# Performance work log

Measured on AMD Instinct MI355X. Metric: run time of the kernel, lower is better.

## Reference

```python
import jax, jax.numpy as jnp
import numpy as np

BN_EPS = 1e-5


def _get_normals(radius, nsample, xyz):
    # xyz: [B, N, 3] -> normals [B, N, 3] (eigenvector of smallest eigenvalue)
    B, N, _ = xyz.shape
    sq = jnp.sum(xyz * xyz, axis=-1)                      # [B, N]
    sqrdists = sq[:, :, None] + sq[:, None, :] - 2.0 * jnp.einsum('bnc,bmc->bnm', xyz, xyz)
    ar = jnp.arange(N, dtype=jnp.int32)
    group_idx = jnp.where(sqrdists > radius * radius, N, ar[None, None, :])  # [B, N, N]
    group_idx = jnp.sort(group_idx, axis=-1)[:, :, :nsample]                 # [B, N, ns]
    group_idx = jnp.where(group_idx == N, group_idx[:, :, :1], group_idx)
    group_points = jax.vmap(lambda pts, idx: pts[idx])(xyz, group_idx)       # [B, N, ns, 3]
    centered = group_points - group_points.mean(axis=2, keepdims=True)
    cov = jnp.einsum('bnsc,bnsd->bncd', centered, centered)                  # [B, N, 3, 3]
    _, eigen_vectors = jnp.linalg.eigh(cov)
    return eigen_vectors[..., 0]


def _conv_bn(h, w, b, g, be, m, v, relu=True):
    # h: [B, N, Cin]; 1x1 Conv1d == per-point linear; BN in eval mode
    h = h @ w.T + b
    h = (h - m) / jnp.sqrt(v + BN_EPS) * g + be
    return jax.nn.relu(h) if relu else h


def setup_inputs() -> dict:
    key = jax.random.key(0)
    ks = jax.random.split(key, 32)
    B, N = 4, 4096
    inp = {
        'x': jax.random.uniform(ks[0], (B, N, 3), dtype=jnp.float32),
        'small': 0.2,
        'large': 0.3,
    }
    chans = [(1, 16), (16, 32), (32, 16), (16, 1)]
    for li, (cin, cout) in enumerate(chans, start=1):
        k = 4 * li
        inp[f'w{li}'] = jax.random.normal(ks[k], (cout, cin), dtype=jnp.float32) * (1.0 / np.sqrt(cin))
        inp[f'b{li}'] = jax.random.normal(ks[k + 1], (cout,), dtype=jnp.float32) * 0.1
        inp[f'g{li}'] = jax.random.uniform(ks[k + 2], (cout,), dtype=jnp.float32) + 0.5
        inp[f'be{li}'] = jax.random.normal(ks[k + 3], (cout,), dtype=jnp.float32) * 0.1
        inp[f'm{li}'] = jnp.zeros((cout,), dtype=jnp.float32)
        inp[f'v{li}'] = jnp.ones((cout,), dtype=jnp.float32)
    return inp


def reference(x, small, large,
              w1, b1, g1, be1, m1, v1,
              w2, b2, g2, be2, m2, v2,
              w3, b3, g3, be3, m3, v3,
              w4, b4, g4, be4, m4, v4):
    xyz = x[:, :, :3]
    small_n = _get_normals(small, 32, xyz)   # [B, N, 3]
    large_n = _get_normals(large, 64, xyz)
    curvature = jnp.linalg.norm((small_n - large_n) * 0.5, axis=2)  # [B, N]
    h = curvature[..., None]                                        # [B, N, 1]
    h = _conv_bn(h, w1, b1, g1, be1, m1, v1)
    h = _conv_bn(h, w2, b2, g2, be2, m2, v2)
    h = _conv_bn(h, w3, b3, g3, be3, m3, v3)
    h = _conv_bn(h, w4, b4, g4, be4, m4, v4, relu=False)
    return h[..., 0]                                                # [B, N]
```

## Files before the change

kernel.cpp:

```cpp
#include <hip/hip_runtime.h>
#include <math.h>

#define BLAS_FMA 1
#define SYR2_VARIANT 0

#define DEV static __device__ __forceinline__

DEV float fA(float a, float b){ return __fadd_rn(a,b); }
DEV float fSb(float a, float b){ return __fsub_rn(a,b); }
DEV float fM(float a, float b){ return __fmul_rn(a,b); }
DEV float fDv(float a, float b){ return __fdiv_rn(a,b); }
DEV float fQ(float a){ return __fsqrt_rn(a); }
DEV float fF(float a, float b, float c){ return __builtin_fmaf(a,b,c); }
DEV float fSGN(float a, float b){ return copysignf(a,b); }

DEV float slapy2f(float x, float y){
  float xa=fabsf(x), ya=fabsf(y);
  float w=fmaxf(xa,ya), z=fminf(xa,ya);
  if (z==0.0f) return w;
  float t=fDv(z,w);
  return fM(w, fQ(fA(1.0f, fM(t,t))));
}

DEV void slartgf(float f, float g, float* c, float* s, float* r){
  const float safmin=1.17549435e-38f;
  const float safmax=8.50705917e+37f;
  const float rtmin=1.08420217e-19f;
  const float rtmax=6.52169543e+18f;
  float f1=fabsf(f), g1=fabsf(g);
  if (g==0.0f){ *c=1.0f; *s=0.0f; *r=f; }
  else if (f==0.0f){ *c=0.0f; *s=fSGN(1.0f,g); *r=g1; }
  else {
    if (f1>rtmin && f1<rtmax && g1>rtmin && g1<rtmax){
      float d=fQ(fA(fM(f,f), fM(g,g)));
      *c=fDv(f1,d);
      *r=fSGN(d,f);
      *s=fDv(g,*r);
    } else {
      float u=fminf(safmax, fmaxf(safmin, fmaxf(f1,g1)));
      float fs=fDv(f,u), gs=fDv(g,u);
      float d=fQ(fA(fM(fs,fs), fM(gs,gs)));
      *c=fDv(fabsf(fs), d);
      *r=fSGN(d,f);
      *s=fDv(gs,*r);
      *r=fM(*r,u);
    }
  }
}

DEV void slaev2f(float a, float b, float c, float* rt1, float* rt2, float* cs1, float* sn1){
  float sm=fA(a,c);
  float df=fSb(a,c);
  float adf=fabsf(df);
  float tb=fA(b,b);
  float ab=fabsf(tb);
  float acmx, acmn;
  if (fabsf(a)>fabsf(c)){ acmx=a; acmn=c; } else { acmx=c; acmn=a; }
  float rt;
  if (adf>ab){ float t=fDv(ab,adf); rt=fM(adf, fQ(fA(1.0f, fM(t,t)))); }
  else if (adf<ab){ float t=fDv(adf,ab); rt=fM(ab, fQ(fA(1.0f, fM(t,t)))); }
  else { rt=fM(ab, fQ(2.0f)); }
  int sgn1;
  if (sm<0.0f){
    *rt1=fM(0.5f, fSb(sm,rt)); sgn1=-1;
    *rt2=fSb(fM(fDv(acmx,*rt1),acmn), fM(fDv(b,*rt1),b));
  } else if (sm>0.0f){
    *rt1=fM(0.5f, fA(sm,rt)); sgn1=1;
    *rt2=fSb(fM(fDv(acmx,*rt1),acmn), fM(fDv(b,*rt1),b));
  } else {
    *rt1=fM(0.5f,rt); *rt2=fM(-0.5f,rt); sgn1=1;
  }
  float cs; int sgn2;
  if (df>=0.0f){ cs=fA(df,rt); sgn2=1; } else { cs=fSb(df,rt); sgn2=-1; }
  float acs=fabsf(cs);
  if (acs>ab){
    float ct=fDv(-tb,cs);
    *sn1=fDv(1.0f, fQ(fA(1.0f, fM(ct,ct))));
    *cs1=fM(ct,*sn1);
  } else {
    if (ab==0.0f){ *cs1=1.0f; *sn1=0.0f; }
    else {
      float tn=fDv(-cs,tb);
      *cs1=fDv(1.0f, fQ(fA(1.0f, fM(tn,tn))));
      *sn1=fM(tn,*cs1);
    }
  }
  if (sgn1==sgn2){ float tn=*cs1; *cs1=-(*sn1); *sn1=tn; }
}

DEV void eig3_smallest(float a00, float a10, float a20, float a11, float a21, float a22,
                       float* vout){
  const float RMIN=3.13916472e-16f;
  const float RMAX=3.18559313e+15f;
  float anrm=fmaxf(fabsf(a00), fmaxf(fabsf(a10), fmaxf(fabsf(a20),
             fmaxf(fabsf(a11), fmaxf(fabsf(a21), fabsf(a22))))));
  if (anrm>0.0f && anrm<RMIN){
    float sig=fDv(RMIN,anrm);
    a00=fM(a00,sig); a10=fM(a10,sig); a20=fM(a20,sig);
    a11=fM(a11,sig); a21=fM(a21,sig); a22=fM(a22,sig);
  } else if (anrm>RMAX){
    float sig=fDv(RMAX,anrm);
    a00=fM(a00,sig); a10=fM(a10,sig); a20=fM(a20,sig);
    a11=fM(a11,sig); a21=fM(a21,sig); a22=fM(a22,sig);
  }
  float d[3], e[2];
  float tau1=0.0f, hv2=0.0f;
  {
    float xnorm=fabsf(a20);
    if (xnorm==0.0f){
      tau1=0.0f;
      d[0]=a00; d[1]=a11; d[2]=a22;
      e[0]=a10; e[1]=a21;
    } else {
      float alpha=a10;
      float beta=-fSGN(slapy2f(alpha,xnorm), alpha);
      tau1=fDv(fSb(beta,alpha), beta);
      float rs=fDv(1.0f, fSb(alpha,beta));
      hv2=fM(a20, rs);
      float t2a=fM(a21, hv2);
#if BLAS_FMA
      float w1=fF(tau1, t2a, fM(tau1, a11));
      float w2=fF(fM(tau1,hv2), a22, fM(tau1, a21));
      float sd=fF(hv2, w2, w1);
#else
      float w1=fA(fM(tau1,a11), fM(tau1,t2a));
      float w2=fA(fM(tau1,a21), fM(fM(tau1,hv2),a22));
      float sd=fA(w1, fM(w2,hv2));
#endif
      float al2=fM(fM(-0.5f,tau1), sd);
      float nw1=fA(w1, al2);
#if BLAS_FMA
      float nw2=fF(al2, hv2, w2);
#else
      float nw2=fA(w2, fM(al2,hv2));
#endif
      w1=nw1; w2=nw2;
      float b11, b21, b22;
#if SYR2_VARIANT==0
      b11=fA(a11, fM(-2.0f, w1));
      b21=fA(a21, fF(hv2, -w1, -w2));
      b22=fA(a22, fF(hv2, -w2, fM(w2, -hv2)));
#elif SYR2_VARIANT==1
      b11=fSb(fSb(a11, w1), w1);
      b21=fSb(fF(hv2, -w1, a21), w2);
      b22=fF(w2, -hv2, fF(hv2, -w2, a22));
#else
      b11=fA(fA(a11, -w1), -w1);
      b21=fA(fA(a21, fM(hv2,-w1)), -w2);
      b22=fA(fA(a22, fM(hv2,-w2)), fM(w2,-hv2));
#endif
      d[0]=a00; d[1]=b11; d[2]=b22;
      e[0]=beta; e[1]=b21;
    }
  }
  float z[9]={1.0f,0.0f,0.0f, 0.0f,1.0f,0.0f, 0.0f,0.0f,1.0f};
  const float EPS=5.96046448e-08f;
  const float EPS2=3.55271368e-15f;
  const float SAFMIN=1.17549435e-38f;
  const float SSFMAX=3.07445735e+18f;
  const float SSFMIN=3.05175781e-05f;
  int l1=1, jtot=0; const int nmaxit=90;
  bool skip_sort=false;
  while (l1<=3){
    if (l1>1) e[l1-2]=0.0f;
    int m=3;
    for (int mm=l1; mm<=2; ++mm){
      float tst=fabsf(e[mm-1]);
      if (tst==0.0f){ m=mm; break; }
      if (tst<=fM(fM(fQ(fabsf(d[mm-1])), fQ(fabsf(d[mm]))), EPS)){ e[mm-1]=0.0f; m=mm; break; }
    }
    int l=l1, lsv=l, lend=m, lendsv=m;
    l1=m+1;
    if (lend==l) continue;
    float anorm=fabsf(d[lend-1]);
    for (int i=l; i<=lend-1; ++i){ anorm=fmaxf(anorm,fabsf(d[i-1])); anorm=fmaxf(anorm,fabsf(e[i-1])); }
    if (anorm==0.0f) continue;
    int iscale=0;
    if (anorm>SSFMAX){
      iscale=1; float mv=fDv(SSFMAX,anorm);
      for (int i=l;i<=lend;++i) d[i-1]=fM(d[i-1],mv);
      for (int i=l;i<=lend-1;++i) e[i-1]=fM(e[i-1],mv);
    } else if (anorm<SSFMIN){
      iscale=2; float mv=fDv(SSFMIN,anorm);
      for (int i=l;i<=lend;++i) d[i-1]=fM(d[i-1],mv);
      for (int i=l;i<=lend-1;++i) e[i-1]=fM(e[i-1],mv);
    }
    if (fabsf(d[lend-1])<fabsf(d[l-1])){ lend=lsv; l=lendsv; }
    if (lend>l){
      for (;;){
        int M=lend;
        if (l!=lend){
          for (int mm=l; mm<=lend-1; ++mm){
            float ee=fabsf(e[mm-1]);
            float tst=fM(ee,ee);
            if (tst<=fA(fM(fM(EPS2,fabsf(d[mm-1])), fabsf(d[mm])), SAFMIN)){ M=mm; break; }
          }
        }
        if (M<lend) e[M-1]=0.0f;
        float p=d[l-1];
        if (M==l){
          l+=1;
          if (l<=lend) continue; else break;
        }
        if (M==l+1){
          float rt1,rt2,cc,ss;
          slaev2f(d[l-1], e[l-1], d[l], &rt1,&rt2,&cc,&ss);
          for (int i=0;i<3;++i){
            float t=z[i+3*l];
            z[i+3*l]    =fSb(fM(cc,t), fM(ss,z[i+3*(l-1)]));
            z[i+3*(l-1)]=fA (fM(ss,t), fM(cc,z[i+3*(l-1)]));
          }
          d[l-1]=rt1; d[l]=rt2; e[l-1]=0.0f; l+=2;
          if (l<=lend) continue; else break;
        }
        if (jtot==nmaxit) break;
        ++jtot;
        float g=fDv(fSb(d[l],p), fM(2.0f,e[l-1]));
        float r=slapy2f(g,1.0f);
        g=fA(fSb(d[M-1],p), fDv(e[l-1], fA(g, fSGN(r,g))));
        float s=1.0f, c=1.0f; p=0.0f;
        float cst[2], sst[2];
        for (int i=M-1; i>=l; --i){
          float f=fM(s,e[i-1]);
          float bb=fM(c,e[i-1]);
          slartgf(g,f,&c,&s,&r);
          if (i!=M-1) e[i]=r;
          g=fSb(d[i],p);
          r=fA(fM(fSb(d[i-1],g),s), fM(fM(2.0f,c),bb));
          p=fM(s,r);
          d[i]=fA(g,p);
          g=fSb(fM(c,r),bb);
          cst[i-l]=c; sst[i-l]=-s;
        }
        int nr=M-l;
        for (int j=nr; j>=1; --j){
          float ct=cst[j-1], st=sst[j-1];
          if (ct!=1.0f || st!=0.0f){
            int c0=(l-1)+(j-1);
            for (int i=0;i<3;++i){
              float t=z[i+3*(c0+1)];
              z[i+3*(c0+1)]=fSb(fM(ct,t), fM(st,z[i+3*c0]));
              z[i+3*c0]    =fA (fM(st,t), fM(ct,z[i+3*c0]));
            }
          }
        }
        d[l-1]=fSb(d[l-1],p);
        e[l-1]=g;
      }
    } else {
      for (;;){
        int M=lend;
        if (l!=lend){
          for (int mm=l; mm>=lend+1; --mm){
            float ee=fabsf(e[mm-2]);
            float tst=fM(ee,ee);
            if (tst<=fA(fM(fM(EPS2,fabsf(d[mm-1])), fabsf(d[mm-2])), SAFMIN)){ M=mm; break; }
          }
        }
        if (M>lend) e[M-2]=0.0f;
        float p=d[l-1];
        if (M==l){
          l-=1;
          if (l>=lend) continue; else break;
        }
        if (M==l-1){
          float rt1,rt2,cc,ss;
          slaev2f(d[l-2], e[l-2], d[l-1], &rt1,&rt2,&cc,&ss);
          for (int i=0;i<3;++i){
            float t=z[i+3*(l-1)];
            z[i+3*(l-1)]=fSb(fM(cc,t), fM(ss,z[i+3*(l-2)]));
            z[i+3*(l-2)]=fA (fM(ss,t), fM(cc,z[i+3*(l-2)]));
          }
          d[l-2]=rt1; d[l-1]=rt2; e[l-2]=0.0f; l-=2;
          if (l>=lend) continue; else break;
        }
        if (jtot==nmaxit) break;
        ++jtot;
        float g=fDv(fSb(d[l-2],p), fM(2.0f,e[l-2]));
        float r=slapy2f(g,1.0f);
        g=fA(fSb(d[M-1],p), fDv(e[l-2], fA(g, fSGN(r,g))));
        float s=1.0f, c=1.0f; p=0.0f;
        float cst[2], sst[2];
        for (int i=M; i<=l-1; ++i){
          float f=fM(s,e[i-1]);
          float bb=fM(c,e[i-1]);
          slartgf(g,f,&c,&s,&r);
          if (i!=M) e[i-2]=r;
          g=fSb(d[i-1],p);
          r=fA(fM(fSb(d[i],g),s), fM(fM(2.0f,c),bb));
          p=fM(s,r);
          d[i-1]=fA(g,p);
          g=fSb(fM(c,r),bb);
          cst[i-M]=c; sst[i-M]=s;
        }
        int nr=l-M;
        for (int j=1; j<=nr; ++j){
          float ct=cst[j-1], st=sst[j-1];
          if (ct!=1.0f || st!=0.0f){
            int c0=(M-1)+(j-1);
            for (int i=0;i<3;++i){
              float t=z[i+3*(c0+1)];
              z[i+3*(c0+1)]=fSb(fM(ct,t), fM(st,z[i+3*c0]));
              z[i+3*c0]    =fA(fM(st,t), fM(ct,z[i+3*c0]));
            }
          }
        }
        d[l-1]=fSb(d[l-1],p);
        e[l-2]=g;
      }
    }
    if (iscale==1){
      float mv=fDv(anorm,SSFMAX);
      for (int i=lsv;i<=lendsv;++i) d[i-1]=fM(d[i-1],mv);
      for (int i=lsv;i<=lendsv-1;++i) e[i-1]=fM(e[i-1],mv);
    } else if (iscale==2){
      float mv=fDv(anorm,SSFMIN);
      for (int i=lsv;i<=lendsv;++i) d[i-1]=fM(d[i-1],mv);
      for (int i=lsv;i<=lendsv-1;++i) e[i-1]=fM(e[i-1],mv);
    }
    if (jtot>=nmaxit){ skip_sort=true; break; }
  }
  if (!skip_sort){
    for (int ii=2; ii<=3; ++ii){
      int i=ii-1, k=i; float p=d[i-1];
      for (int j=ii; j<=3; ++j) if (d[j-1]<p){ k=j; p=d[j-1]; }
      if (k!=i){
        d[k-1]=d[i-1]; d[i-1]=p;
        for (int row=0; row<3; ++row){
          float t=z[row+3*(i-1)]; z[row+3*(i-1)]=z[row+3*(k-1)]; z[row+3*(k-1)]=t;
        }
      }
    }
  }
  float z0=z[0], z1=z[1], z2=z[2];
  if (tau1!=0.0f){
#if BLAS_FMA
    float wv=fF(hv2, z2, z1);
    float t2=fM(-tau1, wv);
    z1=fA(z1, t2);
    z2=fF(t2, hv2, z2);
#else
    float wv=fA(z1, fM(z2,hv2));
    float t2=fM(-tau1, wv);
    z1=fA(z1, t2);
    z2=fA(z2, fM(hv2,t2));
#endif
  }
  vout[0]=z0; vout[1]=z1; vout[2]=z2;
}

struct KP {
  const float* x; const float* rs; const float* rl;
  const float *w1,*b1,*g1,*be1,*m1,*v1;
  const float *w2,*b2,*g2,*be2,*m2,*v2;
  const float *w3,*b3,*g3,*be3,*m3,*v3;
  const float *w4,*b4,*g4,*be4,*m4,*v4;
  float* out;
};

#define WS_STRIDE 128

__global__ __launch_bounds__(64) void scan_kernel(const float* __restrict__ x,
                                                  const float* __restrict__ rsp,
                                                  const float* __restrict__ rlp,
                                                  unsigned short* __restrict__ ws){
  const int lane=threadIdx.x;
  const int pt=blockIdx.x;
  const int b=pt>>12, n=pt&4095;
  const float* P=x+(size_t)b*(4096*3);
  const double rds=rint((double)rsp[0]*1e7)/1e7;
  const double rdl=rint((double)rlp[0]*1e7)/1e7;
  const float rr_s=(float)(rds*rds);
  const float rr_l=(float)(rdl*rdl);
  const float px=P[3*n], py=P[3*n+1], pz=P[3*n+2];
  const float sqn=fA(fA(fM(px,px),fM(py,py)),fM(pz,pz));
  unsigned short* w=ws+(size_t)pt*WS_STRIDE;
  int cs=0, cl=0;
  for (int c=0;c<64;++c){
    int j=c*64+lane;
    float qx=P[3*j], qy=P[3*j+1], qz=P[3*j+2];
    float sqj=fA(fA(fM(qx,qx),fM(qy,qy)),fM(qz,qz));
    float dot=fA(fA(fM(px,qx),fM(py,qy)),fM(pz,qz));
    float d2=fSb(fA(sqn,sqj), fM(2.0f,dot));
    bool pl=!(d2>rr_l);
    bool ps=!(d2>rr_s);
    unsigned long long bl=__ballot(pl);
    unsigned long long bs=__ballot(ps);
    unsigned long long ltm=(1ull<<lane)-1ull;
    int posl=cl+__popcll(bl&ltm);
    int poss=cs+__popcll(bs&ltm);
    if (pl&&posl<64) w[posl]=(unsigned short)j;
    if (ps&&poss<32) w[64+poss]=(unsigned short)j;
    cl+=__popcll(bl); if(cl>64) cl=64;
    cs+=__popcll(bs); if(cs>32) cs=32;
    if (cs>=32&&cl>=64) break;
  }
  if (lane==0){ w[96]=(unsigned short)cl; w[97]=(unsigned short)cs; }
}

__global__ __launch_bounds__(64) void moments_kernel(const float* __restrict__ x,
                                                     const unsigned short* __restrict__ ws,
                                                     float* __restrict__ covB){
  __shared__ float sP[4096*3];
  __shared__ unsigned int sWu[64*65];
  const int lane=threadIdx.x;
  const int base=blockIdx.x*64;
  const int b=base>>12;
  const float* P=x+(size_t)b*(4096*3);
  {
    const float4* src=(const float4*)P;
    float4* dst=(float4*)sP;
    for (int i=lane;i<4096*3/4;i+=64) dst[i]=src[i];
  }
  {
    const unsigned int* wsrc=(const unsigned int*)(ws+(size_t)base*WS_STRIDE);
    for (int i=lane;i<64*64;i+=64){
      int row=i>>6, col=i&63;
      sWu[row*65+col]=wsrc[i];
    }
  }
  __syncthreads();

  const unsigned short* sW16=(const unsigned short*)sWu;
  const int rbase=lane*130;
  const int cln=sW16[rbase+96], csn=sW16[rbase+97];
  const int j0l=sW16[rbase+0],  j0s=sW16[rbase+64];

  float ssx=0.0f,ssy=0.0f,ssz=0.0f, slx=0.0f,sly=0.0f,slz=0.0f;
#pragma unroll 16
  for (int k=0;k<32;++k){
    int idx=(k<csn)?(int)sW16[rbase+64+k]:j0s;
    ssx=fA(ssx,sP[3*idx]); ssy=fA(ssy,sP[3*idx+1]); ssz=fA(ssz,sP[3*idx+2]);
  }
#pragma unroll 16
  for (int k=0;k<64;++k){
    int idx=(k<cln)?(int)sW16[rbase+k]:j0l;
    slx=fA(slx,sP[3*idx]); sly=fA(sly,sP[3*idx+1]); slz=fA(slz,sP[3*idx+2]);
  }
  const float msx=fDv(ssx,32.0f), msy=fDv(ssy,32.0f), msz=fDv(ssz,32.0f);
  const float mlx=fDv(slx,64.0f), mly=fDv(sly,64.0f), mlz=fDv(slz,64.0f);

  float sc0=0,sc1=0,sc2=0,sc3=0,sc4=0,sc5=0;
#pragma unroll 16
  for (int k=0;k<32;++k){
    int idx=(k<csn)?(int)sW16[rbase+64+k]:j0s;
    float cx=fSb(sP[3*idx],msx), cy=fSb(sP[3*idx+1],msy), cz=fSb(sP[3*idx+2],msz);
    sc0=fA(sc0,fM(cx,cx)); sc1=fA(sc1,fM(cy,cx)); sc2=fA(sc2,fM(cz,cx));
    sc3=fA(sc3,fM(cy,cy)); sc4=fA(sc4,fM(cz,cy)); sc5=fA(sc5,fM(cz,cz));
  }
  float lc0=0,lc1=0,lc2=0,lc3=0,lc4=0,lc5=0;
#pragma unroll 16
  for (int k=0;k<64;++k){
    int idx=(k<cln)?(int)sW16[rbase+k]:j0l;
    float cx=fSb(sP[3*idx],mlx), cy=fSb(sP[3*idx+1],mly), cz=fSb(sP[3*idx+2],mlz);
    lc0=fA(lc0,fM(cx,cx)); lc1=fA(lc1,fM(cy,cx)); lc2=fA(lc2,fM(cz,cx));
    lc3=fA(lc3,fM(cy,cy)); lc4=fA(lc4,fM(cz,cy)); lc5=fA(lc5,fM(cz,cz));
  }

  float* cb=covB+(size_t)(base+lane)*12;
  cb[0]=sc0; cb[1]=sc1; cb[2]=sc2; cb[3]=sc3; cb[4]=sc4; cb[5]=sc5;
  cb[6]=lc0; cb[7]=lc1; cb[8]=lc2; cb[9]=lc3; cb[10]=lc4; cb[11]=lc5;
}

__global__ __launch_bounds__(64) void eigmlp_kernel(KP kp, const float* __restrict__ covB){
  __shared__ float sN[32][3];
  const int lane=threadIdx.x;
  const int g=lane>>1;
  const int t=blockIdx.x*32+g;
  const int p=t>>1, which=t&1;
  const float* cb=covB+(size_t)p*12+which*6;
  float v[3];
  eig3_smallest(cb[0],cb[1],cb[2],cb[3],cb[4],cb[5],v);
  if ((lane&1)==0){ sN[g][0]=v[0]; sN[g][1]=v[1]; sN[g][2]=v[2]; }
  __syncthreads();

  if (lane<16){
    const int pt=blockIdx.x*16+lane;
    const float* sn=sN[2*lane];
    const float* ln=sN[2*lane+1];
    float dx=fM(fSb(sn[0],ln[0]),0.5f);
    float dy=fM(fSb(sn[1],ln[1]),0.5f);
    float dz=fM(fSb(sn[2],ln[2]),0.5f);
    float curv=fQ(fA(fA(fM(dx,dx),fM(dy,dy)),fM(dz,dz)));

    float h1[16];
#pragma unroll
    for (int j=0;j<16;++j){
      float a0=fA(fM(kp.w1[j],curv), kp.b1[j]);
      a0=fA(fM(fDv(fSb(a0,kp.m1[j]), fQ(fA(kp.v1[j],1e-5f))), kp.g1[j]), kp.be1[j]);
      h1[j]=fmaxf(a0,0.0f);
    }
    float h2[32];
#pragma unroll
    for (int j=0;j<32;++j){
      float a0=0.0f;
#pragma unroll
      for (int k=0;k<16;++k) a0=fF(h1[k], kp.w2[j*16+k], a0);
      a0=fA(a0, kp.b2[j]);
      a0=fA(fM(fDv(fSb(a0,kp.m2[j]), fQ(fA(kp.v2[j],1e-5f))), kp.g2[j]), kp.be2[j]);
      h2[j]=fmaxf(a0,0.0f);
    }
    float h3[16];
#pragma unroll
    for (int j=0;j<16;++j){
      float a0=0.0f;
#pragma unroll
      for (int k=0;k<32;++k) a0=fF(h2[k], kp.w3[j*32+k], a0);
      a0=fA(a0, kp.b3[j]);
      a0=fA(fM(fDv(fSb(a0,kp.m3[j]), fQ(fA(kp.v3[j],1e-5f))), kp.g3[j]), kp.be3[j]);
      h3[j]=fmaxf(a0,0.0f);
    }
    float o=0.0f;
#pragma unroll
    for (int k=0;k<16;++k) o=fF(h3[k], kp.w4[k], o);
    o=fA(o, kp.b4[0]);
    o=fA(fM(fDv(fSb(o,kp.m4[0]), fQ(fA(kp.v4[0],1e-5f))), kp.g4[0]), kp.be4[0]);
    kp.out[pt]=o;
  }
}

__global__ __launch_bounds__(256) void freq_kernel(KP kp){
  __shared__ float sP[4096*3];
  __shared__ float sSq[4096];
  __shared__ unsigned short sIdxL[64][66];
  __shared__ unsigned short sIdxS[64][34];
  __shared__ unsigned char sCntL[64], sCntS[64];
  const int tid=threadIdx.x;
  const int lane=tid&63, wid=tid>>6;
  const int b=blockIdx.x>>6;
  const int n0=(blockIdx.x&63)*64;
  const float* P=kp.x+(size_t)b*(4096*3);
  for (int i=tid;i<4096*3;i+=256) sP[i]=P[i];
  for (int j=tid;j<4096;j+=256){
    float qx=P[3*j],qy=P[3*j+1],qz=P[3*j+2];
    sSq[j]=fA(fA(fM(qx,qx),fM(qy,qy)),fM(qz,qz));
  }
  __syncthreads();
  const double rds=rint((double)kp.rs[0]*1e7)/1e7;
  const double rdl=rint((double)kp.rl[0]*1e7)/1e7;
  const float rr_s=(float)(rds*rds);
  const float rr_l=(float)(rdl*rdl);
  for (int pi=0; pi<16; ++pi){
    const int pl_i=wid*16+pi;
    const int n=n0+pl_i;
    const float px=sP[3*n], py=sP[3*n+1], pz=sP[3*n+2];
    const float sqn=sSq[n];
    int cs=0, cl=0;
    for (int c=0;c<64;++c){
      int j=c*64+lane;
      float dot=fA(fA(fM(px,sP[3*j]),fM(py,sP[3*j+1])),fM(pz,sP[3*j+2]));
      float d2=fSb(fA(sqn,sSq[j]), fM(2.0f,dot));
      bool pl_=!(d2>rr_l);
      bool ps_=!(d2>rr_s);
      unsigned long long bl=__ballot(pl_);
      unsigned long long bs=__ballot(ps_);
      unsigned long long ltm=(1ull<<lane)-1ull;
      int posl=cl+__popcll(bl&ltm);
      int poss=cs+__popcll(bs&ltm);
      if (pl_&&posl<64) sIdxL[pl_i][posl]=(unsigned short)j;
      if (ps_&&poss<32) sIdxS[pl_i][poss]=(unsigned short)j;
      cl+=__popcll(bl); if(cl>64) cl=64;
      cs+=__popcll(bs); if(cs>32) cs=32;
      if (cs>=32&&cl>=64) break;
    }
    if (lane==0){ sCntL[pl_i]=(unsigned char)cl; sCntS[pl_i]=(unsigned char)cs; }
  }
  __syncthreads();
  if (lane<16){
    const int pl_i=wid*16+lane;
    const int ptg=blockIdx.x*64+pl_i;
    const int csn=sCntS[pl_i], cln=sCntL[pl_i];
    const int j0s=sIdxS[pl_i][0], j0l=sIdxL[pl_i][0];
    float ssx=0.0f,ssy=0.0f,ssz=0.0f, slx=0.0f,sly=0.0f,slz=0.0f;
    for (int k=0;k<32;++k){
      int idx=(k<csn)?(int)sIdxS[pl_i][k]:j0s;
      ssx=fA(ssx,sP[3*idx]); ssy=fA(ssy,sP[3*idx+1]); ssz=fA(ssz,sP[3*idx+2]);
    }
    for (int k=0;k<64;++k){
      int idx=(k<cln)?(int)sIdxL[pl_i][k]:j0l;
      slx=fA(slx,sP[3*idx]); sly=fA(sly,sP[3*idx+1]); slz=fA(slz,sP[3*idx+2]);
    }
    const float msx=fDv(ssx,32.0f), msy=fDv(ssy,32.0f), msz=fDv(ssz,32.0f);
    const float mlx=fDv(slx,64.0f), mly=fDv(sly,64.0f), mlz=fDv(slz,64.0f);
    float sc0=0,sc1=0,sc2=0,sc3=0,sc4=0,sc5=0;
    for (int k=0;k<32;++k){
      int idx=(k<csn)?(int)sIdxS[pl_i][k]:j0s;
      float cx=fSb(sP[3*idx],msx), cy=fSb(sP[3*idx+1],msy), cz=fSb(sP[3*idx+2],msz);
      sc0=fA(sc0,fM(cx,cx)); sc1=fA(sc1,fM(cy,cx)); sc2=fA(sc2,fM(cz,cx));
      sc3=fA(sc3,fM(cy,cy)); sc4=fA(sc4,fM(cz,cy)); sc5=fA(sc5,fM(cz,cz));
    }
    float lc0=0,lc1=0,lc2=0,lc3=0,lc4=0,lc5=0;
    for (int k=0;k<64;++k){
      int idx=(k<cln)?(int)sIdxL[pl_i][k]:j0l;
      float cx=fSb(sP[3*idx],mlx), cy=fSb(sP[3*idx+1],mly), cz=fSb(sP[3*idx+2],mlz);
      lc0=fA(lc0,fM(cx,cx)); lc1=fA(lc1,fM(cy,cx)); lc2=fA(lc2,fM(cz,cx));
      lc3=fA(lc3,fM(cy,cy)); lc4=fA(lc4,fM(cz,cy)); lc5=fA(lc5,fM(cz,cz));
    }
    float snv[3], lnv[3];
    eig3_smallest(sc0,sc1,sc2,sc3,sc4,sc5, snv);
    eig3_smallest(lc0,lc1,lc2,lc3,lc4,lc5, lnv);
    float dx=fM(fSb(snv[0],lnv[0]),0.5f);
    float dy=fM(fSb(snv[1],lnv[1]),0.5f);
    float dz=fM(fSb(snv[2],lnv[2]),0.5f);
    float curv=fQ(fA(fA(fM(dx,dx),fM(dy,dy)),fM(dz,dz)));
    float h1[16];
#pragma unroll
    for (int j=0;j<16;++j){
      float a0=fA(fM(kp.w1[j],curv), kp.b1[j]);
      a0=fA(fM(fDv(fSb(a0,kp.m1[j]), fQ(fA(kp.v1[j],1e-5f))), kp.g1[j]), kp.be1[j]);
      h1[j]=fmaxf(a0,0.0f);
    }
    float h2[32];
#pragma unroll
    for (int j=0;j<32;++j){
      float a0=0.0f;
#pragma unroll
      for (int k=0;k<16;++k) a0=fF(h1[k], kp.w2[j*16+k], a0);
      a0=fA(a0, kp.b2[j]);
      a0=fA(fM(fDv(fSb(a0,kp.m2[j]), fQ(fA(kp.v2[j],1e-5f))), kp.g2[j]), kp.be2[j]);
      h2[j]=fmaxf(a0,0.0f);
    }
    float h3[16];
#pragma unroll
    for (int j=0;j<16;++j){
      float a0=0.0f;
#pragma unroll
      for (int k=0;k<32;++k) a0=fF(h2[k], kp.w3[j*32+k], a0);
      a0=fA(a0, kp.b3[j]);
      a0=fA(fM(fDv(fSb(a0,kp.m3[j]), fQ(fA(kp.v3[j],1e-5f))), kp.g3[j]), kp.be3[j]);
      h3[j]=fmaxf(a0,0.0f);
    }
    float o=0.0f;
#pragma unroll
    for (int k=0;k<16;++k) o=fF(h3[k], kp.w4[k], o);
    o=fA(o, kp.b4[0]);
    o=fA(fM(fDv(fSb(o,kp.m4[0]), fQ(fA(kp.v4[0],1e-5f))), kp.g4[0]), kp.be4[0]);
    kp.out[ptg]=o;
  }
}

extern "C" void kernel_launch(void* const* d_in, const int* in_sizes, int n_in,
                              void* d_out, int out_size, void* d_ws, size_t ws_size,
                              hipStream_t stream){
  (void)n_in; (void)out_size;
  KP kp;
  kp.x  =(const float*)d_in[0];
  kp.rs =(const float*)d_in[1];
  kp.rl =(const float*)d_in[2];
  kp.w1 =(const float*)d_in[3];  kp.b1 =(const float*)d_in[4];  kp.g1 =(const float*)d_in[5];
  kp.be1=(const float*)d_in[6];  kp.m1 =(const float*)d_in[7];  kp.v1 =(const float*)d_in[8];
  kp.w2 =(const float*)d_in[9];  kp.b2 =(const float*)d_in[10]; kp.g2 =(const float*)d_in[11];
  kp.be2=(const float*)d_in[12]; kp.m2 =(const float*)d_in[13]; kp.v2 =(const float*)d_in[14];
  kp.w3 =(const float*)d_in[15]; kp.b3 =(const float*)d_in[16]; kp.g3 =(const float*)d_in[17];
  kp.be3=(const float*)d_in[18]; kp.m3 =(const float*)d_in[19]; kp.v3 =(const float*)d_in[20];
  kp.w4 =(const float*)d_in[21]; kp.b4 =(const float*)d_in[22]; kp.g4 =(const float*)d_in[23];
  kp.be4=(const float*)d_in[24]; kp.m4 =(const float*)d_in[25]; kp.v4 =(const float*)d_in[26];
  kp.out=(float*)d_out;
  const int BN=in_sizes[0]/3;
  const size_t ws_need=(size_t)BN*(256+48);
  if (ws_size>=ws_need){
    unsigned short* wsA=(unsigned short*)d_ws;
    float* covB=(float*)((char*)d_ws + (size_t)BN*256);
    scan_kernel<<<BN, 64, 0, stream>>>(kp.x, kp.rs, kp.rl, wsA);
    moments_kernel<<<BN/64, 64, 0, stream>>>(kp.x, wsA, covB);
    eigmlp_kernel<<<BN/16, 64, 0, stream>>>(kp, covB);
  } else {
    freq_kernel<<<BN/64, 256, 0, stream>>>(kp);
  }
}
```

Baseline: 197.0 us.

## Fuse neighbor scan and covariance moments into one per-point kernel

Merges the scan and moments kernels, so neighbor indices stay in shared memory instead of a global workspace, and computes the means and covariance entries with 6 and 12 lanes per point. It also prefetches the next chunk of candidate points in the scan loop. This removes a kernel launch, the workspace write and read, and the per-block 48KB point-cloud staging. The trade-off is that the moments now run in only a few lanes per wavefront with uncached global gathers, which may serialize work inside each 64-thread block.

```diff
diff --git a/kernel.cpp b/kernel.cpp
--- a/kernel.cpp
+++ b/kernel.cpp
@@ -358,12 +358,14 @@
   float* out;
 };
 
-#define WS_STRIDE 128
-
-__global__ __launch_bounds__(64) void scan_kernel(const float* __restrict__ x,
-                                                  const float* __restrict__ rsp,
-                                                  const float* __restrict__ rlp,
-                                                  unsigned short* __restrict__ ws){
+__global__ __launch_bounds__(64) void scanmom_kernel(const float* __restrict__ x,
+                                                     const float* __restrict__ rsp,
+                                                     const float* __restrict__ rlp,
+                                                     float* __restrict__ covB){
+  __shared__ unsigned short sIdxL[64];
+  __shared__ unsigned short sIdxS[32];
+  __shared__ float sSum[6];
+  __shared__ float sMean[6];
   const int lane=threadIdx.x;
   const int pt=blockIdx.x;
   const int b=pt>>12, n=pt&4095;
@@ -374,13 +376,17 @@
   const float rr_l=(float)(rdl*rdl);
   const float px=P[3*n], py=P[3*n+1], pz=P[3*n+2];
   const float sqn=fA(fA(fM(px,px),fM(py,py)),fM(pz,pz));
-  unsigned short* w=ws+(size_t)pt*WS_STRIDE;
+
   int cs=0, cl=0;
+  float qx=P[3*lane], qy=P[3*lane+1], qz=P[3*lane+2];
   for (int c=0;c<64;++c){
-    int j=c*64+lane;
-    float qx=P[3*j], qy=P[3*j+1], qz=P[3*j+2];
-    float sqj=fA(fA(fM(qx,qx),fM(qy,qy)),fM(qz,qz));
-    float dot=fA(fA(fM(px,qx),fM(py,qy)),fM(pz,qz));
+    float cqx=qx, cqy=qy, cqz=qz;
+    if (c<63){
+      int jn=(c+1)*64+lane;
+      qx=P[3*jn]; qy=P[3*jn+1]; qz=P[3*jn+2];
+    }
+    float sqj=fA(fA(fM(cqx,cqx),fM(cqy,cqy)),fM(cqz,cqz));
+    float dot=fA(fA(fM(px,cqx),fM(py,cqy)),fM(pz,cqz));
     float d2=fSb(fA(sqn,sqj), fM(2.0f,dot));
     bool pl=!(d2>rr_l);
     bool ps=!(d2>rr_s);
@@ -389,77 +395,50 @@
     unsigned long long ltm=(1ull<<lane)-1ull;
     int posl=cl+__popcll(bl&ltm);
     int poss=cs+__popcll(bs&ltm);
-    if (pl&&posl<64) w[posl]=(unsigned short)j;
-    if (ps&&poss<32) w[64+poss]=(unsigned short)j;
+    int jj=c*64+lane;
+    if (pl&&posl<64) sIdxL[posl]=(unsigned short)jj;
+    if (ps&&poss<32) sIdxS[poss]=(unsigned short)jj;
     cl+=__popcll(bl); if(cl>64) cl=64;
     cs+=__popcll(bs); if(cs>32) cs=32;
     if (cs>=32&&cl>=64) break;
   }
-  if (lane==0){ w[96]=(unsigned short)cl; w[97]=(unsigned short)cs; }
-}
-
-__global__ __launch_bounds__(64) void moments_kernel(const float* __restrict__ x,
-                                                     const unsigned short* __restrict__ ws,
-                                                     float* __restrict__ covB){
-  __shared__ float sP[4096*3];
-  __shared__ unsigned int sWu[64*65];
-  const int lane=threadIdx.x;
-  const int base=blockIdx.x*64;
-  const int b=base>>12;
-  const float* P=x+(size_t)b*(4096*3);
-  {
-    const float4* src=(const float4*)P;
-    float4* dst=(float4*)sP;
-    for (int i=lane;i<4096*3/4;i+=64) dst[i]=src[i];
-  }
-  {
-    const unsigned int* wsrc=(const unsigned int*)(ws+(size_t)base*WS_STRIDE);
-    for (int i=lane;i<64*64;i+=64){
-      int row=i>>6, col=i&63;
-      sWu[row*65+col]=wsrc[i];
-    }
-  }
   __syncthreads();
 
-  const unsigned short* sW16=(const unsigned short*)sWu;
-  const int rbase=lane*130;
-  const int cln=sW16[rbase+96], csn=sW16[rbase+97];
-  const int j0l=sW16[rbase+0],  j0s=sW16[rbase+64];
-
-  float ssx=0.0f,ssy=0.0f,ssz=0.0f, slx=0.0f,sly=0.0f,slz=0.0f;
+  if (lane<6){
+    int g=lane/3, ci=lane-3*g;
+    int cnt=g?cl:cs, lim=g?64:32;
+    int j0=g?(int)sIdxL[0]:(int)sIdxS[0];
+    float acc=0.0f;
 #pragma unroll 16
-  for (int k=0;k<32;++k){
-    int idx=(k<csn)?(int)sW16[rbase+64+k]:j0s;
-    ssx=fA(ssx,sP[3*idx]); ssy=fA(ssy,sP[3*idx+1]); ssz=fA(ssz,sP[3*idx+2]);
-  }
+    for (int k=0;k<64;++k){
+      if (k>=lim) break;
+      int idx=(k<cnt)?(g?(int)sIdxL[k]:(int)sIdxS[k]):j0;
+      acc=fA(acc, P[3*idx+ci]);
+    }
+    sSum[lane]=acc;
+  }
+  __syncthreads();
+  if (lane<6) sMean[lane]=fDv(sSum[lane], (lane<3)?32.0f:64.0f);
+  __syncthreads();
+
+  if (lane<12){
+    int g=lane/6, ce=lane-6*g;
+    int a =(ce<3)?ce:((ce==5)?2:(ce-2));
+    int bi=(ce<3)?0 :((ce==5)?2:1);
+    int cnt=g?cl:cs, lim=g?64:32;
+    int j0=g?(int)sIdxL[0]:(int)sIdxS[0];
+    float mA=sMean[g*3+a], mB=sMean[g*3+bi];
+    float acc=0.0f;
 #pragma unroll 16
-  for (int k=0;k<64;++k){
-    int idx=(k<cln)?(int)sW16[rbase+k]:j0l;
-    slx=fA(slx,sP[3*idx]); sly=fA(sly,sP[3*idx+1]); slz=fA(slz,sP[3*idx+2]);
-  }
-  const float msx=fDv(ssx,32.0f), msy=fDv(ssy,32.0f), msz=fDv(ssz,32.0f);
-  const float mlx=fDv(slx,64.0f), mly=fDv(sly,64.0f), mlz=fDv(slz,64.0f);
-
-  float sc0=0,sc1=0,sc2=0,sc3=0,sc4=0,sc5=0;
-#pragma unroll 16
-  for (int k=0;k<32;++k){
-    int idx=(k<csn)?(int)sW16[rbase+64+k]:j0s;
-    float cx=fSb(sP[3*idx],msx), cy=fSb(sP[3*idx+1],msy), cz=fSb(sP[3*idx+2],msz);
-    sc0=fA(sc0,fM(cx,cx)); sc1=fA(sc1,fM(cy,cx)); sc2=fA(sc2,fM(cz,cx));
-    sc3=fA(sc3,fM(cy,cy)); sc4=fA(sc4,fM(cz,cy)); sc5=fA(sc5,fM(cz,cz));
-  }
-  float lc0=0,lc1=0,lc2=0,lc3=0,lc4=0,lc5=0;
-#pragma unroll 16
-  for (int k=0;k<64;++k){
-    int idx=(k<cln)?(int)sW16[rbase+k]:j0l;
-    float cx=fSb(sP[3*idx],mlx), cy=fSb(sP[3*idx+1],mly), cz=fSb(sP[3*idx+2],mlz);
-    lc0=fA(lc0,fM(cx,cx)); lc1=fA(lc1,fM(cy,cx)); lc2=fA(lc2,fM(cz,cx));
-    lc3=fA(lc3,fM(cy,cy)); lc4=fA(lc4,fM(cz,cy)); lc5=fA(lc5,fM(cz,cz));
-  }
-
-  float* cb=covB+(size_t)(base+lane)*12;
-  cb[0]=sc0; cb[1]=sc1; cb[2]=sc2; cb[3]=sc3; cb[4]=sc4; cb[5]=sc5;
-  cb[6]=lc0; cb[7]=lc1; cb[8]=lc2; cb[9]=lc3; cb[10]=lc4; cb[11]=lc5;
+    for (int k=0;k<64;++k){
+      if (k>=lim) break;
+      int idx=(k<cnt)?(g?(int)sIdxL[k]:(int)sIdxS[k]):j0;
+      float va=fSb(P[3*idx+a], mA);
+      float vb=fSb(P[3*idx+bi], mB);
+      acc=fA(acc, fM(va,vb));
+    }
+    covB[(size_t)pt*12+lane]=acc;
+  }
 }
 
 __global__ __launch_bounds__(64) void eigmlp_kernel(KP kp, const float* __restrict__ covB){
@@ -657,12 +636,10 @@
   kp.be4=(const float*)d_in[24]; kp.m4 =(const float*)d_in[25]; kp.v4 =(const float*)d_in[26];
   kp.out=(float*)d_out;
   const int BN=in_sizes[0]/3;
-  const size_t ws_need=(size_t)BN*(256+48);
+  const size_t ws_need=(size_t)BN*48;
   if (ws_size>=ws_need){
-    unsigned short* wsA=(unsigned short*)d_ws;
-    float* covB=(float*)((char*)d_ws + (size_t)BN*256);
-    scan_kernel<<<BN, 64, 0, stream>>>(kp.x, kp.rs, kp.rl, wsA);
-    moments_kernel<<<BN/64, 64, 0, stream>>>(kp.x, wsA, covB);
+    float* covB=(float*)d_ws;
+    scanmom_kernel<<<BN, 64, 0, stream>>>(kp.x, kp.rs, kp.rl, covB);
     eigmlp_kernel<<<BN/16, 64, 0, stream>>>(kp, covB);
   } else {
     freq_kernel<<<BN/64, 256, 0, stream>>>(kp);
```

Result: slower. 210.9 us (+7.1%).

## Fuse moments into eig/MLP kernel and stage scan indices in LDS

Applied to the files above, without the earlier changes.

The separate moments kernel is removed. Its mean and covariance accumulation moves into the eig/MLP kernel, which now splits the work across lanes, one lane per (point, group, component) or covariance element, and reads point coordinates straight from global memory instead of staging the whole 48KB cloud in LDS. The scan kernel now collects neighbor indices in shared memory and writes them out as coalesced 32-bit words. This drops a kernel launch and the covB round trip, and raises parallelism in the moments phase, at the cost of scattered global gathers and branchy per-lane loops.

```diff
diff --git a/kernel.cpp b/kernel.cpp
--- a/kernel.cpp
+++ b/kernel.cpp
@@ -364,6 +364,7 @@
                                                   const float* __restrict__ rsp,
                                                   const float* __restrict__ rlp,
                                                   unsigned short* __restrict__ ws){
+  __shared__ unsigned short sIdx[128];
   const int lane=threadIdx.x;
   const int pt=blockIdx.x;
   const int b=pt>>12, n=pt&4095;
@@ -374,7 +375,6 @@
   const float rr_l=(float)(rdl*rdl);
   const float px=P[3*n], py=P[3*n+1], pz=P[3*n+2];
   const float sqn=fA(fA(fM(px,px),fM(py,py)),fM(pz,pz));
-  unsigned short* w=ws+(size_t)pt*WS_STRIDE;
   int cs=0, cl=0;
   for (int c=0;c<64;++c){
     int j=c*64+lane;
@@ -389,93 +389,97 @@
     unsigned long long ltm=(1ull<<lane)-1ull;
     int posl=cl+__popcll(bl&ltm);
     int poss=cs+__popcll(bs&ltm);
-    if (pl&&posl<64) w[posl]=(unsigned short)j;
-    if (ps&&poss<32) w[64+poss]=(unsigned short)j;
+    if (pl&&posl<64) sIdx[posl]=(unsigned short)j;
+    if (ps&&poss<32) sIdx[64+poss]=(unsigned short)j;
     cl+=__popcll(bl); if(cl>64) cl=64;
     cs+=__popcll(bs); if(cs>32) cs=32;
     if (cs>=32&&cl>=64) break;
   }
-  if (lane==0){ w[96]=(unsigned short)cl; w[97]=(unsigned short)cs; }
-}
-
-__global__ __launch_bounds__(64) void moments_kernel(const float* __restrict__ x,
-                                                     const unsigned short* __restrict__ ws,
-                                                     float* __restrict__ covB){
-  __shared__ float sP[4096*3];
-  __shared__ unsigned int sWu[64*65];
+  if (lane==0){ sIdx[96]=(unsigned short)cl; sIdx[97]=(unsigned short)cs; }
+  __syncthreads();
+  unsigned int* wd=(unsigned int*)(ws+(size_t)pt*WS_STRIDE);
+  const unsigned int* sd=(const unsigned int*)sIdx;
+  if (lane<49) wd[lane]=sd[lane];
+}
+
+__global__ __launch_bounds__(64) void eigmlp_kernel(KP kp, const unsigned short* __restrict__ ws){
+  __shared__ unsigned int sWu[16*65];
+  __shared__ float sSum[96];
+  __shared__ float sCov[192];
+  __shared__ float sN[32][3];
   const int lane=threadIdx.x;
-  const int base=blockIdx.x*64;
+  const int base=blockIdx.x*16;
   const int b=base>>12;
-  const float* P=x+(size_t)b*(4096*3);
-  {
-    const float4* src=(const float4*)P;
-    float4* dst=(float4*)sP;
-    for (int i=lane;i<4096*3/4;i+=64) dst[i]=src[i];
-  }
+  const float* X=kp.x+(size_t)b*(4096*3);
   {
     const unsigned int* wsrc=(const unsigned int*)(ws+(size_t)base*WS_STRIDE);
-    for (int i=lane;i<64*64;i+=64){
+    for (int i=lane;i<16*64;i+=64){
       int row=i>>6, col=i&63;
       sWu[row*65+col]=wsrc[i];
     }
   }
   __syncthreads();
-
   const unsigned short* sW16=(const unsigned short*)sWu;
-  const int rbase=lane*130;
-  const int cln=sW16[rbase+96], csn=sW16[rbase+97];
-  const int j0l=sW16[rbase+0],  j0s=sW16[rbase+64];
-
-  float ssx=0.0f,ssy=0.0f,ssz=0.0f, slx=0.0f,sly=0.0f,slz=0.0f;
+
+  for (int pass=0; pass<2; ++pass){
+    int c=pass*64+lane;
+    if (c<96){
+      int pt=c/6, rem=c-6*pt;
+      int g=rem/3, ci=rem-3*g;
+      const int r130=pt*130;
+      int cnt=g?(int)sW16[r130+96]:(int)sW16[r130+97];
+      int lim=g?64:32;
+      int j0 =g?(int)sW16[r130+0]:(int)sW16[r130+64];
+      float acc=0.0f;
 #pragma unroll 16
-  for (int k=0;k<32;++k){
-    int idx=(k<csn)?(int)sW16[rbase+64+k]:j0s;
-    ssx=fA(ssx,sP[3*idx]); ssy=fA(ssy,sP[3*idx+1]); ssz=fA(ssz,sP[3*idx+2]);
-  }
+      for (int k=0;k<64;++k){
+        if (k>=lim) break;
+        int idx=(k<cnt)?(g?(int)sW16[r130+k]:(int)sW16[r130+64+k]):j0;
+        acc=fA(acc, X[3*idx+ci]);
+      }
+      sSum[c]=acc;
+    }
+  }
+  __syncthreads();
+
+  for (int pass=0; pass<3; ++pass){
+    int c=pass*64+lane;
+    int pt=c/12, ce=c-12*pt;
+    int g=ce/6, cc=ce-6*g;
+    int a =(cc<3)?cc:((cc==5)?2:(cc-2));
+    int bi=(cc<3)?0 :((cc==5)?2:1);
+    const int r130=pt*130;
+    int cnt=g?(int)sW16[r130+96]:(int)sW16[r130+97];
+    int lim=g?64:32;
+    int j0 =g?(int)sW16[r130+0]:(int)sW16[r130+64];
+    float denom=g?64.0f:32.0f;
+    float mA=fDv(sSum[pt*6+g*3+a], denom);
+    float mB=fDv(sSum[pt*6+g*3+bi], denom);
+    float acc=0.0f;
 #pragma unroll 16
-  for (int k=0;k<64;++k){
-    int idx=(k<cln)?(int)sW16[rbase+k]:j0l;
-    slx=fA(slx,sP[3*idx]); sly=fA(sly,sP[3*idx+1]); slz=fA(slz,sP[3*idx+2]);
-  }
-  const float msx=fDv(ssx,32.0f), msy=fDv(ssy,32.0f), msz=fDv(ssz,32.0f);
-  const float mlx=fDv(slx,64.0f), mly=fDv(sly,64.0f), mlz=fDv(slz,64.0f);
-
-  float sc0=0,sc1=0,sc2=0,sc3=0,sc4=0,sc5=0;
-#pragma unroll 16
-  for (int k=0;k<32;++k){
-    int idx=(k<csn)?(int)sW16[rbase+64+k]:j0s;
-    float cx=fSb(sP[3*idx],msx), cy=fSb(sP[3*idx+1],msy), cz=fSb(sP[3*idx+2],msz);
-    sc0=fA(sc0,fM(cx,cx)); sc1=fA(sc1,fM(cy,cx)); sc2=fA(sc2,fM(cz,cx));
-    sc3=fA(sc3,fM(cy,cy)); sc4=fA(sc4,fM(cz,cy)); sc5=fA(sc5,fM(cz,cz));
-  }
-  float lc0=0,lc1=0,lc2=0,lc3=0,lc4=0,lc5=0;
-#pragma unroll 16
-  for (int k=0;k<64;++k){
-    int idx=(k<cln)?(int)sW16[rbase+k]:j0l;
-    float cx=fSb(sP[3*idx],mlx), cy=fSb(sP[3*idx+1],mly), cz=fSb(sP[3*idx+2],mlz);
-    lc0=fA(lc0,fM(cx,cx)); lc1=fA(lc1,fM(cy,cx)); lc2=fA(lc2,fM(cz,cx));
-    lc3=fA(lc3,fM(cy,cy)); lc4=fA(lc4,fM(cz,cy)); lc5=fA(lc5,fM(cz,cz));
-  }
-
-  float* cb=covB+(size_t)(base+lane)*12;
-  cb[0]=sc0; cb[1]=sc1; cb[2]=sc2; cb[3]=sc3; cb[4]=sc4; cb[5]=sc5;
-  cb[6]=lc0; cb[7]=lc1; cb[8]=lc2; cb[9]=lc3; cb[10]=lc4; cb[11]=lc5;
-}
-
-__global__ __launch_bounds__(64) void eigmlp_kernel(KP kp, const float* __restrict__ covB){
-  __shared__ float sN[32][3];
-  const int lane=threadIdx.x;
-  const int g=lane>>1;
-  const int t=blockIdx.x*32+g;
-  const int p=t>>1, which=t&1;
-  const float* cb=covB+(size_t)p*12+which*6;
-  float v[3];
-  eig3_smallest(cb[0],cb[1],cb[2],cb[3],cb[4],cb[5],v);
-  if ((lane&1)==0){ sN[g][0]=v[0]; sN[g][1]=v[1]; sN[g][2]=v[2]; }
+    for (int k=0;k<64;++k){
+      if (k>=lim) break;
+      int idx=(k<cnt)?(g?(int)sW16[r130+k]:(int)sW16[r130+64+k]):j0;
+      float va=fSb(X[3*idx+a], mA);
+      float vb=fSb(X[3*idx+bi], mB);
+      acc=fA(acc, fM(va,vb));
+    }
+    sCov[c]=acc;
+  }
   __syncthreads();
 
+  {
+    const int g2=lane>>1;
+    const int p=g2>>1, which=g2&1;
+    const float* cb=&sCov[p*12+which*6];
+    float v[3];
+    eig3_smallest(cb[0],cb[1],cb[2],cb[3],cb[4],cb[5],v);
+    if ((lane&1)==0){ sN[g2][0]=v[0]; sN[g2][1]=v[1]; sN[g2][2]=v[2]; }
+  }
+  __syncthreads();
+
   if (lane<16){
-    const int pt=blockIdx.x*16+lane;
+    const int pt=base+lane;
     const float* sn=sN[2*lane];
     const float* ln=sN[2*lane+1];
     float dx=fM(fSb(sn[0],ln[0]),0.5f);
@@ -657,13 +661,11 @@
   kp.be4=(const float*)d_in[24]; kp.m4 =(const float*)d_in[25]; kp.v4 =(const float*)d_in[26];
   kp.out=(float*)d_out;
   const int BN=in_sizes[0]/3;
-  const size_t ws_need=(size_t)BN*(256+48);
+  const size_t ws_need=(size_t)BN*256;
   if (ws_size>=ws_need){
     unsigned short* wsA=(unsigned short*)d_ws;
-    float* covB=(float*)((char*)d_ws + (size_t)BN*256);
     scan_kernel<<<BN, 64, 0, stream>>>(kp.x, kp.rs, kp.rl, wsA);
-    moments_kernel<<<BN/64, 64, 0, stream>>>(kp.x, wsA, covB);
-    eigmlp_kernel<<<BN/16, 64, 0, stream>>>(kp, covB);
+    eigmlp_kernel<<<BN/16, 64, 0, stream>>>(kp, wsA);
   } else {
     freq_kernel<<<BN/64, 256, 0, stream>>>(kp);
   }
```

New measurement: 206.9 us. 5.0% more time.
